# Performance work log

Hardware: AMD Instinct MI355X
Metric: run time of the kernel (lower is better)

Reference implementation:

```python
import jax, jax.numpy as jnp
import numpy as np

M = 6            # num posenc frequencies
K0 = -3
WIDTH = 128
DEPTH = 7
N_PTS = 131072
N_ANNEAL = 0.6 * 5000.0   # self.N = 0.6 * max_iter
PI = 3.14                 # module uses literal 3.14, not math.pi


def _linear_init(key, fan_in, fan_out):
    k1, k2 = jax.random.split(key)
    lim = 1.0 / np.sqrt(fan_in)
    W = jax.random.uniform(k1, (fan_out, fan_in), jnp.float32, -lim, lim)
    b = jax.random.uniform(k2, (fan_out,), jnp.float32, -lim, lim)
    return W, b


def setup_inputs() -> dict:
    key = jax.random.key(0)
    ks = jax.random.split(key, 11)
    dim_x = M * 6 + 3  # 39
    W_in, b_in = _linear_init(ks[0], dim_x, WIDTH)
    hw, hb = [], []
    for i in range(DEPTH - 1):
        W, b = _linear_init(ks[1 + i], WIDTH, WIDTH)
        hw.append(W)
        hb.append(b)
    Ws, bs = jnp.stack(hw), jnp.stack(hb)  # [6,128,128], [6,128]
    Ww, bw = _linear_init(ks[7], WIDTH, 3)
    Wv, bv = _linear_init(ks[8], WIDTH, 3)
    x = jax.random.normal(ks[9], (N_PTS, 3), jnp.float32)
    return {"x": x, "W_in": W_in, "b_in": b_in, "Ws": Ws, "bs": bs,
            "Ww": Ww, "bw": bw, "Wv": Wv, "bv": bv, "iter": 2500}


def _posenc(pos, it):
    # pos: [N,3]
    j = jnp.arange(M, dtype=pos.dtype)
    a = M * it / N_ANNEAL
    w_a = (1.0 - jnp.cos(jnp.clip(a - j, 0.0, 1.0) * PI)) * 0.5      # [M]
    mul = (2.0 ** (j + K0)) * PI                                     # [M]
    ang = pos[..., :, None] * mul                                    # [N,3,M]
    sin = jnp.sin(ang) * w_a
    cos = jnp.cos(ang) * w_a
    # order: sinx,cosx,siny,cosy,sinz,cosz -> [N,3,2,M] flattened
    code = jnp.stack([sin, cos], axis=-2).reshape(pos.shape[0], 6 * M)
    return jnp.concatenate([pos, code], axis=-1)                     # [N,3+6M]


def _skew(w):
    z = jnp.zeros_like(w[..., 0])
    return jnp.stack([
        jnp.stack([z, -w[..., 2], w[..., 1]], -1),
        jnp.stack([w[..., 2], z, -w[..., 0]], -1),
        jnp.stack([-w[..., 1], w[..., 0], z], -1)], -2)              # [N,3,3]


def _exp_se3(w, v, theta):
    # w,v: [N,3] (axis and v/theta), theta: [N,1]
    W = _skew(w)
    W2 = W @ W
    th = theta[..., None]                                            # [N,1,1]
    s, c = jnp.sin(th), jnp.cos(th)
    I = jnp.eye(3, dtype=w.dtype)
    R = I + s * W + (1.0 - c) * W2
    G = I * th + (1.0 - c) * W + (th - s) * W2
    t = G @ v[..., None]                                             # [N,3,1]
    return R, t


def _warp(x, it, W_in, b_in, Ws, bs, Ww, bw, Wv, bv):
    fea = _posenc(x, it)
    fea = jax.nn.leaky_relu(fea @ W_in.T + b_in, 0.01)

    def layer(f, Wb):
        W, b = Wb
        return jax.nn.relu(f @ W.T + b), None

    fea, _ = jax.lax.scan(layer, fea, (Ws, bs))
    w = fea @ Ww.T + bw
    v = fea @ Wv.T + bv
    theta = jnp.linalg.norm(w, axis=-1, keepdims=True)
    w = w / theta
    v = v / theta
    R, t = _exp_se3(w, v, theta)
    return (R @ x[..., None] + t)[..., 0]                            # [N,3]


def reference(x, W_in, b_in, Ws, bs, Ww, bw, Wv, bv, iter):
    it = float(iter)
    warped = _warp(x, it, W_in, b_in, Ws, bs, Ww, bw, Wv, bv)
    # jacobian of sum over batch -> [3, N, 3]; transpose -> [N, 3, 3]
    f_sum = lambda xx: _warp(xx, it, W_in, b_in, Ws, bs, Ww, bw, Wv, bv).sum(0)
    J = jnp.transpose(jax.jacrev(f_sum)(x), (1, 0, 2))
    return warped, J
```

## Files before the change

### kernel.cpp

```cpp
#include <hip/hip_runtime.h>
#include <math.h>

#define NPTS    131072
#define PPB     64
#define THREADS 256
#define NBLK    (NPTS / PPB)
#define HOFF    (7 * 16384)
#define HSZ     (32 * 128)

typedef __attribute__((ext_vector_type(8)))  short short8;
typedef __attribute__((ext_vector_type(16))) float f32x16;
typedef __attribute__((ext_vector_type(2)))  short s16x2;
typedef __attribute__((ext_vector_type(2)))  __bf16 bf16x2v;

union b8cv { short8 v; unsigned u[4]; };

__device__ __forceinline__ unsigned short f2bf(float f) {
  unsigned u = __float_as_uint(f);
  unsigned r = (u + 0x7fffu + ((u >> 16) & 1u)) >> 16;
  return (unsigned short)r;
}
__device__ __forceinline__ unsigned pk2(float lo, float hi) {
  bf16x2v t;
  t[0] = (__bf16)lo;
  t[1] = (__bf16)hi;
  unsigned u; __builtin_memcpy(&u, &t, 4); return u;
}
__device__ __forceinline__ void gld16(const unsigned short* g, unsigned short* l) {
  __builtin_amdgcn_global_load_lds(
      (const __attribute__((address_space(1))) unsigned int*)(g),
      (__attribute__((address_space(3))) unsigned int*)(l), 16, 0, 0);
}
__device__ __forceinline__ f32x16 zf() {
  f32x16 z;
  #pragma unroll
  for (int e = 0; e < 16; ++e) z[e] = 0.0f;
  return z;
}
__device__ __forceinline__ float qbcast0(float v) {
  return __int_as_float(
      __builtin_amdgcn_mov_dpp(__float_as_int(v), 0x000, 0xf, 0xf, true));
}
__device__ __forceinline__ unsigned relu_pk(unsigned p) {
  unsigned vs = (unsigned)__builtin_amdgcn_mov_dpp((int)p, 0x000, 0xf, 0xf, true);
  s16x2 m2; __builtin_memcpy(&m2, &vs, 4);
  m2 = m2 >> 15;
  unsigned m; __builtin_memcpy(&m, &m2, 4);
  unsigned r;
  asm("v_bfi_b32 %0, %1, 0, %2" : "=v"(r) : "v"(m), "v"(p));
  return r;
}
__device__ __forceinline__ void cross3(const float a[3], const float b[3], float o[3]) {
  o[0] = a[1]*b[2] - a[2]*b[1];
  o[1] = a[2]*b[0] - a[0]*b[2];
  o[2] = a[0]*b[1] - a[1]*b[0];
}
__device__ __forceinline__ float dot3(const float a[3], const float b[3]) {
  return a[0]*b[0] + a[1]*b[1] + a[2]*b[2];
}

__global__ void convert_weights(const float* __restrict__ W_in,
                                const float* __restrict__ b_in,
                                const float* __restrict__ Ws,
                                const float* __restrict__ bs,
                                const float* __restrict__ Ww,
                                const float* __restrict__ Wv,
                                unsigned short* __restrict__ wsW) {
  int idx = blockIdx.x * 256 + threadIdx.x;
  if (idx >= HOFF + HSZ) return;
  float v;
  if (idx < HOFF) {
    int l = idx >> 14, r = idx & 16383, c = r >> 7, k = r & 127;
    if (l == 0) {
      if (k < 39) {
        v = W_in[c * 39 + k];
      } else if (k >= 64 && c < 14) {
        int j  = c * 64 + (k - 64);
        int lb = j >> 7, rr = j & 127;
        int mt = rr >> 5, rd = rr & 31;
        int e2 = rd & 3, hh = (rd >> 2) & 1, q = rd >> 3;
        int src = 32*mt + 16*(q>>1) + 8*hh + 4*(q&1) + e2;
        v = (lb == 0) ? b_in[src] : bs[(lb - 1) * 128 + src];
      } else {
        v = 0.0f;
      }
    } else {
      v = Ws[(l - 1) * 16384 + c * 128 + k];
    }
  } else {
    int r = idx - HOFF, o = r >> 7, k = r & 127;
    v = (o < 3) ? Ww[o * 128 + k] : (o < 6) ? Wv[(o - 3) * 128 + k] : 0.0f;
  }
  wsW[idx] = f2bf(v);
}

__device__ __forceinline__ void dma_full(const unsigned short* __restrict__ g,
                                         unsigned short* lds, int tid) {
  #pragma unroll
  for (int i = 0; i < 8; ++i) {
    int flat = i * 256 + tid;
    int R = flat >> 4, chs = flat & 15, ch = chs ^ (R & 15);
    gld16(g + R * 128 + ch * 8, lds + flat * 8);
  }
}

__device__ __forceinline__ short8 bias_af(const unsigned short* __restrict__ bb,
                                          int off, int c32) {
  b8cv cv;
  cv.u[0] = (unsigned)bb[off + c32];
  cv.u[1] = 0; cv.u[2] = 0; cv.u[3] = 0;
  return cv.v;
}

template <bool LEAKY>
__device__ __forceinline__ void act_pack(const f32x16 (&acc)[2], short8* dst) {
  #pragma unroll
  for (int mt = 0; mt < 2; ++mt)
    #pragma unroll
    for (int qh = 0; qh < 2; ++qh) {
      b8cv cv;
      #pragma unroll
      for (int qs = 0; qs < 2; ++qs) {
        int q = 2*qh + qs;
        if (LEAKY) {
          float pr[4];
          #pragma unroll
          for (int e2 = 0; e2 < 4; ++e2) {
            float post = acc[mt][4*q + e2];
            float vraw = qbcast0(post);
            pr[e2] = vraw > 0.0f ? post : post * 0.01f;
          }
          cv.u[2*qs]     = pk2(pr[0], pr[1]);
          cv.u[2*qs + 1] = pk2(pr[2], pr[3]);
        } else {
          cv.u[2*qs]     = relu_pk(pk2(acc[mt][4*q+0], acc[mt][4*q+1]));
          cv.u[2*qs + 1] = relu_pk(pk2(acc[mt][4*q+2], acc[mt][4*q+3]));
        }
      }
      dst[2*mt + qh] = cv.v;
    }
}

template <int NKS, bool LEAKY, bool HASNEXT>
__device__ __forceinline__ void mlp_layer(short8 (&pgA)[8], short8 (&pgB)[8],
                                          const unsigned short* scur,
                                          unsigned short* snxt,
                                          const int (&aoff)[8],
                                          const unsigned short* __restrict__ bb,
                                          const short8 bind,
                                          const unsigned short* __restrict__ Wnext,
                                          int tid, int c32) {
  if (HASNEXT) dma_full(Wnext, snxt, tid);

  short8 tA[4], tB[4];

  {
    f32x16 aA[2], aB[2];
    __builtin_amdgcn_s_setprio(1);
    #pragma unroll
    for (int m = 0; m < 2; ++m) {
      f32x16 bias = __builtin_amdgcn_mfma_f32_32x32x16_bf16(
          bias_af(bb, 64 + 32*m, c32), bind, zf(), 0, 0, 0);
      short8 af0 = *(const short8*)(scur + m * 4096 + aoff[0]);
      aA[m] = __builtin_amdgcn_mfma_f32_32x32x16_bf16(af0, pgA[0], bias, 0, 0, 0);
      aB[m] = __builtin_amdgcn_mfma_f32_32x32x16_bf16(af0, pgB[0], bias, 0, 0, 0);
    }
    #pragma unroll
    for (int ks = 1; ks < NKS; ++ks) {
      #pragma unroll
      for (int m = 0; m < 2; ++m) {
        short8 af = *(const short8*)(scur + m * 4096 + aoff[ks]);
        aA[m] = __builtin_amdgcn_mfma_f32_32x32x16_bf16(af, pgA[ks], aA[m], 0, 0, 0);
        aB[m] = __builtin_amdgcn_mfma_f32_32x32x16_bf16(af, pgB[ks], aB[m], 0, 0, 0);
      }
    }
    __builtin_amdgcn_s_setprio(0);
    act_pack<LEAKY>(aA, tA);
    act_pack<LEAKY>(aB, tB);
  }

  {
    f32x16 aA[2], aB[2];
    __builtin_amdgcn_s_setprio(1);
    #pragma unroll
    for (int m = 0; m < 2; ++m) {
      f32x16 bias = __builtin_amdgcn_mfma_f32_32x32x16_bf16(
          bias_af(bb, 192 + 32*m, c32), bind, zf(), 0, 0, 0);
      short8 af0 = *(const short8*)(scur + (2 + m) * 4096 + aoff[0]);
      aA[m] = __builtin_amdgcn_mfma_f32_32x32x16_bf16(af0, pgA[0], bias, 0, 0, 0);
      aB[m] = __builtin_amdgcn_mfma_f32_32x32x16_bf16(af0, pgB[0], bias, 0, 0, 0);
    }
    #pragma unroll
    for (int ks = 1; ks < NKS; ++ks) {
      #pragma unroll
      for (int m = 0; m < 2; ++m) {
        short8 af = *(const short8*)(scur + (2 + m) * 4096 + aoff[ks]);
        aA[m] = __builtin_amdgcn_mfma_f32_32x32x16_bf16(af, pgA[ks], aA[m], 0, 0, 0);
        aB[m] = __builtin_amdgcn_mfma_f32_32x32x16_bf16(af, pgB[ks], aB[m], 0, 0, 0);
      }
    }
    __builtin_amdgcn_s_setprio(0);
    act_pack<LEAKY>(aA, &pgA[4]);
    act_pack<LEAKY>(aB, &pgB[4]);
  }

  #pragma unroll
  for (int i = 0; i < 4; ++i) { pgA[i] = tA[i]; pgB[i] = tB[i]; }

  if (HASNEXT) __syncthreads();
}

struct SK { int cls, a, t, jf; };
__device__ __forceinline__ constexpr SK slotk(int c) {
  return (c < 3)   ? SK{1, c, 0, 0}
       : (c >= 39) ? SK{0, 0, 0, 0}
       : SK{2, (c-3)/12, ((c-3)%12)/6, ((c-3)%12)%6};
}
__device__ __forceinline__ constexpr float e2sf(int jf) {
  return (float)(1 << jf) * 0.125f * 0.49974652f;
}
__device__ __forceinline__ float eval_slot(SK k, const float (&X)[3],
                                           float sv, float cvv,
                                           const float (&wjv)[6],
                                           const float (&mjw)[6],
                                           float f_d0, const float (&fea)[3]) {
  if (k.cls == 0) return 0.0f;
  if (k.cls == 1) return X[k.a] * f_d0 + fea[k.a];
  float pv = (k.t ? cvv : sv) * wjv[k.jf];
  float pt = (k.t ? -sv : cvv) * mjw[k.jf];
  return pv * f_d0 + pt * fea[k.a];
}

__device__ __forceinline__ void posenc_pack(const float (&X)[3], int h,
                                            const float (&wjv)[6],
                                            const float (&mjw)[6],
                                            float f_d0, const float (&fea)[3],
                                            short8* pg) {
  const bool hI = (h != 0);
  #pragma unroll
  for (int j = 4; j < 8; ++j) pg[j] = (short8)0;
  #pragma unroll
  for (int j = 0; j < 4; ++j) {
    b8cv cv;
    #pragma unroll
    for (int ii = 0; ii < 4; ++ii) {
      int i = 4*j + ii;
      int mt = i >> 3, rr = i & 7, q = rr >> 1, s = rr & 1;
      int u0 = 32*mt + 16*(q>>1) + 4*(q&1) + 2*s;
      float vp[2];
      #pragma unroll
      for (int ci = 0; ci < 2; ++ci) {
        const SK k0 = slotk(u0 + ci);
        const SK k1 = slotk(u0 + ci + 8);
        float rev0 = (k0.cls == 2) ? X[k0.a] * e2sf(k0.jf) : 0.0f;
        float rev1 = (k1.cls == 2) ? X[k1.a] * e2sf(k1.jf) : 0.0f;
        float rev  = hI ? rev1 : rev0;
        float fr   = rev - floorf(rev);
        float sv   = __builtin_amdgcn_sinf(fr);
        float cvv  = __builtin_amdgcn_cosf(fr);
        float v0 = eval_slot(k0, X, sv, cvv, wjv, mjw, f_d0, fea);
        float v1 = eval_slot(k1, X, sv, cvv, wjv, mjw, f_d0, fea);
        vp[ci] = hI ? v1 : v0;
      }
      cv.u[ii] = pk2(vp[0], vp[1]);
    }
    pg[j] = cv.v;
  }
}

__global__ __launch_bounds__(THREADS, 2)
void nerfies_mfma(const float* __restrict__ x,
                  const float* __restrict__ bw,
                  const float* __restrict__ bv,
                  const unsigned short* __restrict__ wsW,
                  const int* __restrict__ iterp,
                  float* __restrict__ out)
{
  __shared__ __align__(16) unsigned short sWl[2][128 * 128];
  float* sH = (float*)sWl[1];

  const int tid  = threadIdx.x;
  const int lane = tid & 63;
  const int wv   = tid >> 6;
  const int c32  = lane & 31;
  const int h    = lane >> 5;
  const int p0   = blockIdx.x * PPB;
  const int sig  = (c32 & 0x13) | ((c32 & 4) << 1) | ((c32 & 8) >> 1);

  dma_full(wsW, sWl[0], tid);

  int aoff[8];
  #pragma unroll
  for (int ks = 0; ks < 8; ++ks) aoff[ks] = ((2*ks + h) ^ (sig & 15)) << 3;
  const unsigned short* s0s = sWl[0] + sig * 128;
  const unsigned short* s1s = sWl[1] + sig * 128;

  short8 bind;
  {
    b8cv cv;
    cv.u[0] = ((c32 & 3) == 0) ? 0x3F00u : 0u;
    cv.u[1] = 0; cv.u[2] = 0; cv.u[3] = 0;
    bind = cv.v;
  }

  const int d   = c32 & 3;
  const int gpA = p0 + wv * 16 + (c32 >> 2);
  const int gpB = gpA + 8;
  float XA[3] = { x[gpA * 3 + 0], x[gpA * 3 + 1], x[gpA * 3 + 2] };
  float XB[3] = { x[gpB * 3 + 0], x[gpB * 3 + 1], x[gpB * 3 + 2] };

  int iraw = iterp[0];
  float it = (iraw > 0 && iraw < 100000000) ? (float)iraw : ((const float*)iterp)[0];
  const float aM = 6.0f * it / 3000.0f;

  float wjv[6], mjw[6];
  #pragma unroll
  for (int jf = 0; jf < 6; ++jf) {
    float e2 = (float)(1 << jf) * 0.125f;
    float tt = fminf(fmaxf(aM - (float)jf, 0.0f), 1.0f);
    float wj = (1.0f - __builtin_amdgcn_cosf(tt * 0.49974652f)) * 0.5f;
    wjv[jf] = wj;
    mjw[jf] = (e2 * 3.14f) * wj;
  }
  const float f_d0 = (d == 0) ? 1.0f : 0.0f;
  const float fea[3] = { (d == 1) ? 1.0f : 0.0f,
                         (d == 2) ? 1.0f : 0.0f,
                         (d == 3) ? 1.0f : 0.0f };

  short8 pgA[8], pgB[8];
  posenc_pack(XA, h, wjv, mjw, f_d0, fea, pgA);
  posenc_pack(XB, h, wjv, mjw, f_d0, fea, pgB);
  __syncthreads();

  mlp_layer<3, true , true >(pgA, pgB, s0s, sWl[1], aoff, wsW + 0*256, bind, wsW + 1*16384, tid, c32);
  mlp_layer<8, false, true >(pgA, pgB, s1s, sWl[0], aoff, wsW + 1*256, bind, wsW + 2*16384, tid, c32);
  mlp_layer<8, false, true >(pgA, pgB, s0s, sWl[1], aoff, wsW + 2*256, bind, wsW + 3*16384, tid, c32);
  mlp_layer<8, false, true >(pgA, pgB, s1s, sWl[0], aoff, wsW + 3*256, bind, wsW + 4*16384, tid, c32);
  mlp_layer<8, false, true >(pgA, pgB, s0s, sWl[1], aoff, wsW + 4*256, bind, wsW + 5*16384, tid, c32);
  mlp_layer<8, false, true >(pgA, pgB, s1s, sWl[0], aoff, wsW + 5*256, bind, wsW + 6*16384, tid, c32);
  mlp_layer<8, false, false>(pgA, pgB, s0s, sWl[1], aoff, wsW + 6*256, bind, wsW,           tid, c32);

  {
    const unsigned short* hw = wsW + HOFF;
    short8 af0 = *(const short8*)(hw + c32 * 128 + 8 * h);
    f32x16 hA = __builtin_amdgcn_mfma_f32_32x32x16_bf16(af0, pgA[0], zf(), 0, 0, 0);
    f32x16 hB = __builtin_amdgcn_mfma_f32_32x32x16_bf16(af0, pgB[0], zf(), 0, 0, 0);
    #pragma unroll
    for (int ks = 1; ks < 8; ++ks) {
      short8 afrag = *(const short8*)(hw + c32 * 128 + ks * 16 + 8 * h);
      hA = __builtin_amdgcn_mfma_f32_32x32x16_bf16(afrag, pgA[ks], hA, 0, 0, 0);
      hB = __builtin_amdgcn_mfma_f32_32x32x16_bf16(afrag, pgB[ks], hB, 0, 0, 0);
    }
    int rgA = wv * 64 + c32;
    int rgB = rgA + 32;
    if (h == 0) {
      *(float4*)(sH + rgA * 8) = make_float4(hA[0], hA[1], hA[2], hA[3]);
      *(float4*)(sH + rgB * 8) = make_float4(hB[0], hB[1], hB[2], hB[3]);
    } else {
      *(float2*)(sH + rgA * 8 + 4) = make_float2(hA[0], hA[1]);
      *(float2*)(sH + rgB * 8 + 4) = make_float2(hB[0], hB[1]);
    }
  }
  __syncthreads();

  {
    const int pd  = lane & 15;
    const int sel = lane >> 4;
    const int gpp = p0 + wv * 16 + pd;
    const int rb  = wv * 64 + (pd >> 3) * 32 + (pd & 7) * 4;
    float XX[3] = { x[gpp*3+0], x[gpp*3+1], x[gpp*3+2] };
    float w[3], v[3];
    #pragma unroll
    for (int i = 0; i < 3; ++i) {
      w[i] = sH[rb * 8 + i]     + bw[i];
      v[i] = sH[rb * 8 + 3 + i] + bv[i];
    }
    float th  = sqrtf(w[0]*w[0] + w[1]*w[1] + w[2]*w[2]);
    float ith = 1.0f / th;
    float u[3]  = { w[0]*ith, w[1]*ith, w[2]*ith };
    float vh[3] = { v[0]*ith, v[1]*ith, v[2]*ith };
    float s = sinf(th), c = cosf(th);
    float C2 = 1.0f - c;
    float ths = th - s;
    float uxx[3]; cross3(u, XX, uxx);
    float udx = dot3(u, XX);
    float uxv[3]; cross3(u, vh, uxv);
    float udv = dot3(u, vh);
    if (sel == 3) {
      #pragma unroll
      for (int i = 0; i < 3; ++i) {
        float Rx = XX[i] + s * uxx[i] + C2 * (u[i] * udx - XX[i]);
        float tt = th * vh[i] + C2 * uxv[i] + ths * (u[i] * udv - vh[i]);
        out[gpp*3 + i] = Rx + tt;
      }
    } else {
      const int dd = sel;
      float* Jout = out + (size_t)NPTS * 3 + (size_t)gpp * 9;
      float dwv[3], dvv[3];
      #pragma unroll
      for (int i = 0; i < 3; ++i) {
        dwv[i] = sH[(rb + 1 + dd) * 8 + i];
        dvv[i] = sH[(rb + 1 + dd) * 8 + 3 + i];
      }
      float dth = dot3(w, dwv) * ith;
      float du[3], dvhv[3];
      #pragma unroll
      for (int i = 0; i < 3; ++i) {
        du[i]   = (dwv[i] - u[i]  * dth) * ith;
        dvhv[i] = (dvv[i] - vh[i] * dth) * ith;
      }
      float ex[3] = { dd == 0 ? 1.0f : 0.0f, dd == 1 ? 1.0f : 0.0f, dd == 2 ? 1.0f : 0.0f };
      float u_dd  = dd == 0 ? u[0] : (dd == 1 ? u[1] : u[2]);
      float dsv  = c  * dth;
      float dC2  = s  * dth;
      float dths = C2 * dth;
      float duxx[3]; cross3(du, XX, duxx);
      float uxe[3];  cross3(u, ex, uxe);
      float dudx = dot3(du, XX) + u_dd;
      float duxv[3]; cross3(du, vh, duxv);
      float uxdv[3]; cross3(u, dvhv, uxdv);
      float dudv = dot3(du, vh) + dot3(u, dvhv);
      #pragma unroll
      for (int i = 0; i < 3; ++i) {
        float dRx = ex[i] + dsv * uxx[i] + s * (duxx[i] + uxe[i])
                  + dC2 * (u[i] * udx - XX[i])
                  + C2 * (du[i] * udx + u[i] * dudx - ex[i]);
        float dt  = dth * vh[i] + th * dvhv[i] + dC2 * uxv[i]
                  + C2 * (duxv[i] + uxdv[i])
                  + dths * (u[i] * udv - vh[i])
                  + ths * (du[i] * udv + u[i] * dudv - dvhv[i]);
        Jout[i * 3 + dd] = dRx + dt;
      }
    }
  }
}

extern "C" void kernel_launch(void* const* d_in, const int* in_sizes, int n_in,
                              void* d_out, int out_size, void* d_ws, size_t ws_size,
                              hipStream_t stream) {
  const float* x    = (const float*)d_in[0];
  const float* W_in = (const float*)d_in[1];
  const float* b_in = (const float*)d_in[2];
  const float* Ws   = (const float*)d_in[3];
  const float* bs   = (const float*)d_in[4];
  const float* Ww   = (const float*)d_in[5];
  const float* bw   = (const float*)d_in[6];
  const float* Wv   = (const float*)d_in[7];
  const float* bv   = (const float*)d_in[8];
  const int*   itp  = (const int*)d_in[9];
  unsigned short* wsW = (unsigned short*)d_ws;

  convert_weights<<<dim3((HOFF + HSZ + 255) / 256), dim3(256), 0, stream>>>(
      W_in, b_in, Ws, bs, Ww, Wv, wsW);
  nerfies_mfma<<<dim3(NBLK), dim3(THREADS), 0, stream>>>(
      x, bw, bv, wsW, itp, (float*)d_out);
}
```

Measured before the change: 181.0 us.

## Halve points per block and split weight staging into half-tiles for higher occupancy

Cuts each block from 64 to 32 points, dropping the second B accumulator set, and shrinks the LDS weight buffer to two 64-row halves. Each layer's weights are now streamed in two halves with an extra barrier between them, and launch bounds are raised to allow three blocks per CU. The aim is to free registers and LDS so more waves can hide latency. The cost is twice as many blocks, each reloading every weight from global memory, more barriers per layer, and less MFMA work per A-fragment load.

```diff
diff --git a/kernel.cpp b/kernel.cpp
--- a/kernel.cpp
+++ b/kernel.cpp
@@ -2,7 +2,7 @@
 #include <math.h>
 
 #define NPTS    131072
-#define PPB     64
+#define PPB     32
 #define THREADS 256
 #define NBLK    (NPTS / PPB)
 #define HOFF    (7 * 16384)
@@ -94,10 +94,10 @@
   wsW[idx] = f2bf(v);
 }
 
-__device__ __forceinline__ void dma_full(const unsigned short* __restrict__ g,
+__device__ __forceinline__ void dma_half(const unsigned short* __restrict__ g,
                                          unsigned short* lds, int tid) {
   #pragma unroll
-  for (int i = 0; i < 8; ++i) {
+  for (int i = 0; i < 4; ++i) {
     int flat = i * 256 + tid;
     int R = flat >> 4, chs = flat & 15, ch = chs ^ (R & 15);
     gld16(g + R * 128 + ch * 8, lds + flat * 8);
@@ -142,72 +142,70 @@
 }
 
 template <int NKS, bool LEAKY, bool HASNEXT>
-__device__ __forceinline__ void mlp_layer(short8 (&pgA)[8], short8 (&pgB)[8],
-                                          const unsigned short* scur,
-                                          unsigned short* snxt,
+__device__ __forceinline__ void mlp_layer(short8 (&pg)[8],
+                                          const unsigned short* s0s,
+                                          const unsigned short* s1s,
+                                          unsigned short* s0w, unsigned short* s1w,
                                           const int (&aoff)[8],
                                           const unsigned short* __restrict__ bb,
                                           const short8 bind,
+                                          const unsigned short* __restrict__ Wthis,
                                           const unsigned short* __restrict__ Wnext,
                                           int tid, int c32) {
-  if (HASNEXT) dma_full(Wnext, snxt, tid);
-
-  short8 tA[4], tB[4];
+  dma_half(Wthis + 64 * 128, s1w, tid);
+
+  short8 t[4];
 
   {
-    f32x16 aA[2], aB[2];
+    f32x16 a[2];
     __builtin_amdgcn_s_setprio(1);
     #pragma unroll
     for (int m = 0; m < 2; ++m) {
       f32x16 bias = __builtin_amdgcn_mfma_f32_32x32x16_bf16(
           bias_af(bb, 64 + 32*m, c32), bind, zf(), 0, 0, 0);
-      short8 af0 = *(const short8*)(scur + m * 4096 + aoff[0]);
-      aA[m] = __builtin_amdgcn_mfma_f32_32x32x16_bf16(af0, pgA[0], bias, 0, 0, 0);
-      aB[m] = __builtin_amdgcn_mfma_f32_32x32x16_bf16(af0, pgB[0], bias, 0, 0, 0);
+      short8 af0 = *(const short8*)(s0s + m * 4096 + aoff[0]);
+      a[m] = __builtin_amdgcn_mfma_f32_32x32x16_bf16(af0, pg[0], bias, 0, 0, 0);
     }
     #pragma unroll
     for (int ks = 1; ks < NKS; ++ks) {
       #pragma unroll
       for (int m = 0; m < 2; ++m) {
-        short8 af = *(const short8*)(scur + m * 4096 + aoff[ks]);
-        aA[m] = __builtin_amdgcn_mfma_f32_32x32x16_bf16(af, pgA[ks], aA[m], 0, 0, 0);
-        aB[m] = __builtin_amdgcn_mfma_f32_32x32x16_bf16(af, pgB[ks], aB[m], 0, 0, 0);
+        short8 af = *(const short8*)(s0s + m * 4096 + aoff[ks]);
+        a[m] = __builtin_amdgcn_mfma_f32_32x32x16_bf16(af, pg[ks], a[m], 0, 0, 0);
       }
     }
     __builtin_amdgcn_s_setprio(0);
-    act_pack<LEAKY>(aA, tA);
-    act_pack<LEAKY>(aB, tB);
-  }
+    act_pack<LEAKY>(a, t);
+  }
+
+  __syncthreads();
+  if (HASNEXT) dma_half(Wnext, s0w, tid);
 
   {
-    f32x16 aA[2], aB[2];
+    f32x16 a[2];
     __builtin_amdgcn_s_setprio(1);
     #pragma unroll
     for (int m = 0; m < 2; ++m) {
       f32x16 bias = __builtin_amdgcn_mfma_f32_32x32x16_bf16(
           bias_af(bb, 192 + 32*m, c32), bind, zf(), 0, 0, 0);
-      short8 af0 = *(const short8*)(scur + (2 + m) * 4096 + aoff[0]);
-      aA[m] = __builtin_amdgcn_mfma_f32_32x32x16_bf16(af0, pgA[0], bias, 0, 0, 0);
-      aB[m] = __builtin_amdgcn_mfma_f32_32x32x16_bf16(af0, pgB[0], bias, 0, 0, 0);
+      short8 af0 = *(const short8*)(s1s + m * 4096 + aoff[0]);
+      a[m] = __builtin_amdgcn_mfma_f32_32x32x16_bf16(af0, pg[0], bias, 0, 0, 0);
     }
     #pragma unroll
     for (int ks = 1; ks < NKS; ++ks) {
       #pragma unroll
       for (int m = 0; m < 2; ++m) {
-        short8 af = *(const short8*)(scur + (2 + m) * 4096 + aoff[ks]);
-        aA[m] = __builtin_amdgcn_mfma_f32_32x32x16_bf16(af, pgA[ks], aA[m], 0, 0, 0);
-        aB[m] = __builtin_amdgcn_mfma_f32_32x32x16_bf16(af, pgB[ks], aB[m], 0, 0, 0);
+        short8 af = *(const short8*)(s1s + m * 4096 + aoff[ks]);
+        a[m] = __builtin_amdgcn_mfma_f32_32x32x16_bf16(af, pg[ks], a[m], 0, 0, 0);
       }
     }
     __builtin_amdgcn_s_setprio(0);
-    act_pack<LEAKY>(aA, &pgA[4]);
-    act_pack<LEAKY>(aB, &pgB[4]);
-  }
-
-  #pragma unroll
-  for (int i = 0; i < 4; ++i) { pgA[i] = tA[i]; pgB[i] = tB[i]; }
-
-  if (HASNEXT) __syncthreads();
+    act_pack<LEAKY>(a, &pg[4]);
+  }
+
+  #pragma unroll
+  for (int i = 0; i < 4; ++i) pg[i] = t[i];
+  __syncthreads();
 }
 
 struct SK { int cls, a, t, jf; };
@@ -268,7 +266,7 @@
   }
 }
 
-__global__ __launch_bounds__(THREADS, 2)
+__global__ __launch_bounds__(THREADS, 3)
 void nerfies_mfma(const float* __restrict__ x,
                   const float* __restrict__ bw,
                   const float* __restrict__ bv,
@@ -276,7 +274,7 @@
                   const int* __restrict__ iterp,
                   float* __restrict__ out)
 {
-  __shared__ __align__(16) unsigned short sWl[2][128 * 128];
+  __shared__ __align__(16) unsigned short sWl[2][64 * 128];
   float* sH = (float*)sWl[1];
 
   const int tid  = threadIdx.x;
@@ -287,7 +285,7 @@
   const int p0   = blockIdx.x * PPB;
   const int sig  = (c32 & 0x13) | ((c32 & 4) << 1) | ((c32 & 8) >> 1);
 
-  dma_full(wsW, sWl[0], tid);
+  dma_half(wsW, sWl[0], tid);
 
   int aoff[8];
   #pragma unroll
@@ -303,11 +301,9 @@
     bind = cv.v;
   }
 
-  const int d   = c32 & 3;
-  const int gpA = p0 + wv * 16 + (c32 >> 2);
-  const int gpB = gpA + 8;
-  float XA[3] = { x[gpA * 3 + 0], x[gpA * 3 + 1], x[gpA * 3 + 2] };
-  float XB[3] = { x[gpB * 3 + 0], x[gpB * 3 + 1], x[gpB * 3 + 2] };
+  const int d  = c32 & 3;
+  const int gp = p0 + wv * 8 + (c32 >> 2);
+  float X[3] = { x[gp * 3 + 0], x[gp * 3 + 1], x[gp * 3 + 2] };
 
   int iraw = iterp[0];
   float it = (iraw > 0 && iraw < 100000000) ? (float)iraw : ((const float*)iterp)[0];
@@ -327,47 +323,41 @@
                          (d == 2) ? 1.0f : 0.0f,
                          (d == 3) ? 1.0f : 0.0f };
 
-  short8 pgA[8], pgB[8];
-  posenc_pack(XA, h, wjv, mjw, f_d0, fea, pgA);
-  posenc_pack(XB, h, wjv, mjw, f_d0, fea, pgB);
+  short8 pg[8];
+  posenc_pack(X, h, wjv, mjw, f_d0, fea, pg);
   __syncthreads();
 
-  mlp_layer<3, true , true >(pgA, pgB, s0s, sWl[1], aoff, wsW + 0*256, bind, wsW + 1*16384, tid, c32);
-  mlp_layer<8, false, true >(pgA, pgB, s1s, sWl[0], aoff, wsW + 1*256, bind, wsW + 2*16384, tid, c32);
-  mlp_layer<8, false, true >(pgA, pgB, s0s, sWl[1], aoff, wsW + 2*256, bind, wsW + 3*16384, tid, c32);
-  mlp_layer<8, false, true >(pgA, pgB, s1s, sWl[0], aoff, wsW + 3*256, bind, wsW + 4*16384, tid, c32);
-  mlp_layer<8, false, true >(pgA, pgB, s0s, sWl[1], aoff, wsW + 4*256, bind, wsW + 5*16384, tid, c32);
-  mlp_layer<8, false, true >(pgA, pgB, s1s, sWl[0], aoff, wsW + 5*256, bind, wsW + 6*16384, tid, c32);
-  mlp_layer<8, false, false>(pgA, pgB, s0s, sWl[1], aoff, wsW + 6*256, bind, wsW,           tid, c32);
+  mlp_layer<3, true , true >(pg, s0s, s1s, sWl[0], sWl[1], aoff, wsW + 0*256, bind, wsW + 0*16384, wsW + 1*16384, tid, c32);
+  mlp_layer<8, false, true >(pg, s0s, s1s, sWl[0], sWl[1], aoff, wsW + 1*256, bind, wsW + 1*16384, wsW + 2*16384, tid, c32);
+  mlp_layer<8, false, true >(pg, s0s, s1s, sWl[0], sWl[1], aoff, wsW + 2*256, bind, wsW + 2*16384, wsW + 3*16384, tid, c32);
+  mlp_layer<8, false, true >(pg, s0s, s1s, sWl[0], sWl[1], aoff, wsW + 3*256, bind, wsW + 3*16384, wsW + 4*16384, tid, c32);
+  mlp_layer<8, false, true >(pg, s0s, s1s, sWl[0], sWl[1], aoff, wsW + 4*256, bind, wsW + 4*16384, wsW + 5*16384, tid, c32);
+  mlp_layer<8, false, true >(pg, s0s, s1s, sWl[0], sWl[1], aoff, wsW + 5*256, bind, wsW + 5*16384, wsW + 6*16384, tid, c32);
+  mlp_layer<8, false, false>(pg, s0s, s1s, sWl[0], sWl[1], aoff, wsW + 6*256, bind, wsW + 6*16384, wsW,           tid, c32);
 
   {
     const unsigned short* hw = wsW + HOFF;
     short8 af0 = *(const short8*)(hw + c32 * 128 + 8 * h);
-    f32x16 hA = __builtin_amdgcn_mfma_f32_32x32x16_bf16(af0, pgA[0], zf(), 0, 0, 0);
-    f32x16 hB = __builtin_amdgcn_mfma_f32_32x32x16_bf16(af0, pgB[0], zf(), 0, 0, 0);
+    f32x16 hacc = __builtin_amdgcn_mfma_f32_32x32x16_bf16(af0, pg[0], zf(), 0, 0, 0);
     #pragma unroll
     for (int ks = 1; ks < 8; ++ks) {
       short8 afrag = *(const short8*)(hw + c32 * 128 + ks * 16 + 8 * h);
-      hA = __builtin_amdgcn_mfma_f32_32x32x16_bf16(afrag, pgA[ks], hA, 0, 0, 0);
-      hB = __builtin_amdgcn_mfma_f32_32x32x16_bf16(afrag, pgB[ks], hB, 0, 0, 0);
-    }
-    int rgA = wv * 64 + c32;
-    int rgB = rgA + 32;
+      hacc = __builtin_amdgcn_mfma_f32_32x32x16_bf16(afrag, pg[ks], hacc, 0, 0, 0);
+    }
+    int rg = wv * 32 + c32;
     if (h == 0) {
-      *(float4*)(sH + rgA * 8) = make_float4(hA[0], hA[1], hA[2], hA[3]);
-      *(float4*)(sH + rgB * 8) = make_float4(hB[0], hB[1], hB[2], hB[3]);
+      *(float4*)(sH + rg * 8) = make_float4(hacc[0], hacc[1], hacc[2], hacc[3]);
     } else {
-      *(float2*)(sH + rgA * 8 + 4) = make_float2(hA[0], hA[1]);
-      *(float2*)(sH + rgB * 8 + 4) = make_float2(hB[0], hB[1]);
+      *(float2*)(sH + rg * 8 + 4) = make_float2(hacc[0], hacc[1]);
     }
   }
   __syncthreads();
 
-  {
-    const int pd  = lane & 15;
-    const int sel = lane >> 4;
-    const int gpp = p0 + wv * 16 + pd;
-    const int rb  = wv * 64 + (pd >> 3) * 32 + (pd & 7) * 4;
+  if (lane < 32) {
+    const int pd  = lane & 7;
+    const int sel = lane >> 3;
+    const int gpp = p0 + wv * 8 + pd;
+    const int rb  = wv * 32 + pd * 4;
     float XX[3] = { x[gpp*3+0], x[gpp*3+1], x[gpp*3+2] };
     float w[3], v[3];
     #pragma unroll
```

After: 195.6 us. 1.08x slower.
